# Performance work log

Hardware: AMD Instinct MI355X
Metric: run time of the kernel (lower is better)

## Reference

```python
import jax, jax.numpy as jnp
import numpy as np

N = 100000   # nodes
E = 1600000  # edges (avg degree 16)
D = 128      # feature width (constant across the 3 blocks)
L = 3        # number of residual LEConv blocks
EPS = 1e-5
SLOPE = 0.01  # leaky_relu negative slope


def setup_inputs() -> dict:
    key = jax.random.key(0)
    ks = jax.random.split(key, 10)
    y = jax.random.normal(ks[0], (N, D), dtype=jnp.float32)
    edge_index = jax.random.randint(ks[1], (2, E), 0, N, dtype=jnp.int64)
    s = 0.05
    W1 = jax.random.normal(ks[2], (L, D, D), dtype=jnp.float32) * s
    b1 = jax.random.normal(ks[3], (L, D), dtype=jnp.float32) * s
    W2 = jax.random.normal(ks[4], (L, D, D), dtype=jnp.float32) * s   # lin2: no bias
    W3 = jax.random.normal(ks[5], (L, D, D), dtype=jnp.float32) * s
    b3 = jax.random.normal(ks[6], (L, D), dtype=jnp.float32) * s
    ln_w = jnp.ones((L, D), dtype=jnp.float32)
    ln_b = jnp.zeros((L, D), dtype=jnp.float32)
    return {"y": y, "edge_index": edge_index, "W1": W1, "b1": b1,
            "W2": W2, "W3": W3, "b3": b3, "ln_w": ln_w, "ln_b": ln_b}


def reference(y, edge_index, W1, b1, W2, W3, b3, ln_w, ln_b):
    n = y.shape[0]
    src, dst = edge_index[0], edge_index[1]
    # in-degree per destination node (edge_weight = 1)
    deg = jax.ops.segment_sum(jnp.ones((src.shape[0],), dtype=y.dtype), dst,
                              num_segments=n)  # [N]
    for l in range(L):
        # LEConv: out_i = sum_{j->i} (lin1(x)_j - lin2(x)_i) + lin3(x)_i
        a = y @ W1[l] + b1[l]          # [N, D] (lin1, with bias)
        b = y @ W2[l]                  # [N, D] (lin2, no bias)
        agg = jax.ops.segment_sum(a[src], dst, num_segments=n) - deg[:, None] * b
        h = agg + y @ W3[l] + b3[l]    # + lin3(x)
        # PyG LayerNorm mode='graph', batch=None: scalar mean/std over all elems
        h = h - h.mean()
        h = h / (h.std() + EPS)
        h = h * ln_w[l] + ln_b[l]
        # leaky_relu, dropout p=0 (no-op), identity residual
        h = jnp.where(h >= 0, h, SLOPE * h)
        y = y + h
    return y
```

## Files before the change

kernel.cpp:

```cpp
#include <hip/hip_runtime.h>
#include <hip/hip_bf16.h>
#include <math.h>

#define N_NODES 100000
#define N_EDGES 1600000
#define DF      128
#define EPSV    1e-5f
#define SLOPE   0.01f
#define M_TOT   (N_NODES * DF)

#define HG    512
#define EPB   (N_EDGES / HG)
#define NBIN  391

typedef __hip_bfloat16 bf16;
typedef __attribute__((ext_vector_type(8))) short short8;
typedef __attribute__((ext_vector_type(4))) float f32x4;

__global__ void k_detect(const unsigned int* __restrict__ yw32, int* __restrict__ flagp)
{
    __shared__ int cnt;
    if (threadIdx.x == 0) cnt = 0;
    __syncthreads();
    unsigned w = yw32[threadIdx.x];
    int e = (w >> 7) & 0xFF;
    if (e >= 96 && e <= 140) atomicAdd(&cnt, 1);
    __syncthreads();
    if (threadIdx.x == 0) flagp[0] = (cnt >= 150) ? 1 : 0;
}

__global__ void k_zero(int* __restrict__ p, int n)
{
    int i = blockIdx.x * 256 + threadIdx.x;
    if (i < n) p[i] = 0;
}

__device__ __forceinline__ void edge_decode(const int* __restrict__ ei, int e,
                                            int& s, int& d)
{
    bool is64 = ((ei[1] | ei[3] | ei[5] | ei[7]) == 0);
    if (is64) { s = ei[2 * e]; d = ei[2 * (N_EDGES + e)]; }
    else      { s = ei[e];     d = ei[N_EDGES + e];       }
}

__global__ __launch_bounds__(256) void k_hist(
    const void* __restrict__ yin, bf16* __restrict__ yw,
    const int* __restrict__ flagp, const int* __restrict__ ei,
    int* __restrict__ histG)
{
    __shared__ int h[NBIN];
    const int tid = threadIdx.x, b = blockIdx.x;
    for (int i = tid; i < NBIN; i += 256) h[i] = 0;
    __syncthreads();

    const int e0 = b * EPB;
    for (int e = e0 + tid; e < e0 + EPB; e += 256) {
        int s, d;
        edge_decode(ei, e, s, d);
        if ((unsigned)s < N_NODES && (unsigned)d < N_NODES)
            atomicAdd(&h[d >> 8], 1);
    }

    const int isbf = flagp[0];
    for (long t = (long)b * 256 + tid; t < (M_TOT / 8); t += (long)HG * 256) {
        float f[8];
        if (isbf) {
            uint4 v = reinterpret_cast<const uint4*>(yin)[t];
            const bf16* sp = reinterpret_cast<const bf16*>(&v);
#pragma unroll
            for (int j = 0; j < 8; ++j) f[j] = __bfloat162float(sp[j]);
        } else {
            float4 v0 = reinterpret_cast<const float4*>(yin)[2 * t];
            float4 v1 = reinterpret_cast<const float4*>(yin)[2 * t + 1];
            f[0] = v0.x; f[1] = v0.y; f[2] = v0.z; f[3] = v0.w;
            f[4] = v1.x; f[5] = v1.y; f[6] = v1.z; f[7] = v1.w;
        }
        uint4 ov;
        bf16* o = reinterpret_cast<bf16*>(&ov);
#pragma unroll
        for (int j = 0; j < 8; ++j) {
            float x = f[j];
            if (!isfinite(x)) x = 0.f;
            o[j] = __float2bfloat16(x);
        }
        reinterpret_cast<uint4*>(yw)[t] = ov;
    }

    __syncthreads();
    for (int i = tid; i < NBIN; i += 256) histG[i * HG + b] = h[i];
}

__global__ void k_hscan1(int* __restrict__ histG, int* __restrict__ binTotal)
{
    __shared__ int sc[512];
    const int bin = blockIdx.x, tid = threadIdx.x;
    int v = histG[bin * HG + tid];
    sc[tid] = v;
    __syncthreads();
    for (int off = 1; off < 512; off <<= 1) {
        int t = (tid >= off) ? sc[tid - off] : 0;
        __syncthreads();
        sc[tid] += t;
        __syncthreads();
    }
    histG[bin * HG + tid] = sc[tid] - v;
    if (tid == 511) binTotal[bin] = sc[511];
}

__global__ void k_hscan2(const int* __restrict__ binTotal, int* __restrict__ binStart)
{
    __shared__ int sc[512];
    int tid = threadIdx.x;
    int v = (tid < NBIN) ? binTotal[tid] : 0;
    sc[tid] = v;
    __syncthreads();
    for (int off = 1; off < 512; off <<= 1) {
        int t = (tid >= off) ? sc[tid - off] : 0;
        __syncthreads();
        sc[tid] += t;
        __syncthreads();
    }
    if (tid < NBIN) binStart[tid] = sc[tid] - v;
}

__global__ __launch_bounds__(256) void k_scatter(
    const int* __restrict__ ei, const int* __restrict__ histG,
    const int* __restrict__ binStart, int* __restrict__ binned)
{
    __shared__ int base[NBIN];
    __shared__ int cur[NBIN];
    const int tid = threadIdx.x, b = blockIdx.x;
    for (int i = tid; i < NBIN; i += 256) {
        base[i] = binStart[i] + histG[i * HG + b];
        cur[i]  = 0;
    }
    __syncthreads();

    const int e0 = b * EPB;
    for (int e = e0 + tid; e < e0 + EPB; e += 256) {
        int s, d;
        edge_decode(ei, e, s, d);
        if ((unsigned)s < N_NODES && (unsigned)d < N_NODES) {
            int bin = d >> 8;
            int r = atomicAdd(&cur[bin], 1);
            binned[base[bin] + r] = ((d & 255) << 17) | s;
        }
    }
}

__global__ __launch_bounds__(256) void k_bin(
    const int* __restrict__ binned, const int* __restrict__ binStart,
    const int* __restrict__ binTotal, int* __restrict__ edst,
    int* __restrict__ degcnt, int* __restrict__ offs)
{
    __shared__ int hloc[256];
    __shared__ int lofs[256];
    __shared__ int sc[256];
    const int bin = blockIdx.x, tid = threadIdx.x;
    const int bbase = binStart[bin], cnt = binTotal[bin];

    hloc[tid] = 0;
    __syncthreads();
    for (int i = tid; i < cnt; i += 256)
        atomicAdd(&hloc[binned[bbase + i] >> 17], 1);
    __syncthreads();

    const int deg = hloc[tid];
    sc[tid] = deg;
    __syncthreads();
    for (int off = 1; off < 256; off <<= 1) {
        int t = (tid >= off) ? sc[tid - off] : 0;
        __syncthreads();
        sc[tid] += t;
        __syncthreads();
    }
    const int ex = sc[tid] - deg;
    lofs[tid] = ex;
    const int node = bin * 256 + tid;
    if (node < N_NODES) {
        degcnt[node] = deg;
        offs[node]   = bbase + ex;
    }
    hloc[tid] = 0;
    __syncthreads();

    for (int i = tid; i < cnt; i += 256) {
        int v = binned[bbase + i];
        int n = v >> 17;
        int r = atomicAdd(&hloc[n], 1);
        edst[bbase + lofs[n] + r] = v & 0x1FFFF;
    }
}

__global__ void k_wt(const void* __restrict__ W1, const void* __restrict__ W2,
                     const void* __restrict__ W3, bf16* __restrict__ Wt,
                     const int* __restrict__ flagp)
{
    int idx = blockIdx.x * 256 + threadIdx.x;
    const int isbf = flagp[0];
    int mat = idx >> 14;
    int r   = idx & 16383;
    int k   = r >> 7, n = r & 127;
    int l = mat / 3, which = mat - l * 3;
    const void* src = (which == 0) ? W1 : (which == 1 ? W2 : W3);
    size_t ofs = (size_t)l * 16384 + (size_t)k * 128 + n;
    float v = isbf ? __bfloat162float(reinterpret_cast<const bf16*>(src)[ofs])
                   : reinterpret_cast<const float*>(src)[ofs];
    if (!isfinite(v)) v = 0.f;
    Wt[((size_t)mat << 14) + (size_t)n * 128 + k] = __float2bfloat16(v);
}

__global__ void k_small(const void* __restrict__ b1, const void* __restrict__ b3,
                        const void* __restrict__ lnw, const void* __restrict__ lnb,
                        bf16* __restrict__ prm, const int* __restrict__ flagp)
{
    int i = blockIdx.x * 256 + threadIdx.x;
    if (i >= 1536) return;
    const int isbf = flagp[0];
    int which = i / 384, r = i - which * 384;
    const void* src = (which == 0) ? b1 : (which == 1) ? b3 : (which == 2) ? lnw : lnb;
    float v = isbf ? __bfloat162float(reinterpret_cast<const bf16*>(src)[r])
                   : reinterpret_cast<const float*>(src)[r];
    if (!isfinite(v)) v = 0.f;
    prm[i] = __float2bfloat16(v);
}

__global__ __launch_bounds__(256) void k_gemm3(
    bf16* __restrict__ yw, const bf16* __restrict__ hprev,
    const float* __restrict__ stats, const bf16* __restrict__ Wt,
    const bf16* __restrict__ prm, const int* __restrict__ degcnt,
    bf16* __restrict__ aBuf, bf16* __restrict__ cmb, int layer)
{
    __shared__ bf16 Asm[64][136];
    __shared__ bf16 Bsm[128][136];

    const int tid = threadIdx.x;
    const long r0 = (long)blockIdx.x * 64;

    const uint4* gy = reinterpret_cast<const uint4*>(yw);

    if (layer == 0) {
#pragma unroll
        for (int it = 0; it < 4; ++it) {
            int chunk = it * 256 + tid;
            int row = chunk >> 4, colc = (chunk & 15) * 8;
            uint4 v = make_uint4(0, 0, 0, 0);
            long grow = r0 + row;
            if (grow < N_NODES) v = gy[grow * 16 + (chunk & 15)];
            *reinterpret_cast<uint4*>(&Asm[row][colc]) = v;
        }
    } else {
        const float mean = stats[(layer - 1) * 2];
        const float inv  = stats[(layer - 1) * 2 + 1];
        const bf16* lnwc = prm + 768  + (layer - 1) * 128;
        const bf16* lnbc = prm + 1152 + (layer - 1) * 128;
        const uint4* gh = reinterpret_cast<const uint4*>(hprev);
#pragma unroll
        for (int it = 0; it < 4; ++it) {
            int chunk = it * 256 + tid;
            int row = chunk >> 4, c16 = chunk & 15, colc = c16 * 8;
            long grow = r0 + row;
            uint4 ov = make_uint4(0, 0, 0, 0);
            if (grow < N_NODES) {
                uint4 hv = gh[grow * 16 + c16];
                uint4 yv = gy[grow * 16 + c16];
                const bf16* h8 = reinterpret_cast<const bf16*>(&hv);
                const bf16* y8 = reinterpret_cast<const bf16*>(&yv);
                bf16* o8 = reinterpret_cast<bf16*>(&ov);
#pragma unroll
                for (int jj = 0; jj < 8; ++jj) {
                    float g = __bfloat162float(lnwc[colc + jj]);
                    float b = __bfloat162float(lnbc[colc + jj]);
                    float hh = (__bfloat162float(h8[jj]) - mean) * inv * g + b;
                    hh = (hh >= 0.f) ? hh : SLOPE * hh;
                    o8[jj] = __float2bfloat16(__bfloat162float(y8[jj]) + hh);
                }
                reinterpret_cast<uint4*>(yw)[grow * 16 + c16] = ov;
            }
            *reinterpret_cast<uint4*>(&Asm[row][colc]) = ov;
        }
    }

#define STAGE_B(MATIDX)                                                          \
    {                                                                            \
        const uint4* gw = reinterpret_cast<const uint4*>(Wt + ((size_t)(MATIDX) << 14)); \
        _Pragma("unroll")                                                        \
        for (int it = 0; it < 8; ++it) {                                         \
            int chunk = it * 256 + tid;                                          \
            *reinterpret_cast<uint4*>(&Bsm[chunk >> 4][(chunk & 15) * 8]) = gw[chunk]; \
        }                                                                        \
    }

    const int wave = tid >> 6, lane = tid & 63;
    const int lm = lane & 15, quad = lane >> 4;
    const int mrow = wave * 16 + lm;

    f32x4 accB[8], accC[8];
#pragma unroll
    for (int nt = 0; nt < 8; ++nt) {
        accB[nt] = (f32x4){0.f, 0.f, 0.f, 0.f};
        accC[nt] = (f32x4){0.f, 0.f, 0.f, 0.f};
    }

    STAGE_B(layer * 3 + 1);
    __syncthreads();
#pragma unroll
    for (int kk = 0; kk < 4; ++kk) {
        const int kb = kk * 32 + quad * 8;
        short8 afr = *reinterpret_cast<const short8*>(&Asm[mrow][kb]);
#pragma unroll
        for (int nt = 0; nt < 8; ++nt) {
            short8 bfr = *reinterpret_cast<const short8*>(&Bsm[nt * 16 + lm][kb]);
            accB[nt] = __builtin_amdgcn_mfma_f32_16x16x32_bf16(afr, bfr, accB[nt], 0, 0, 0);
        }
    }
    __syncthreads();

    STAGE_B(layer * 3 + 2);
    __syncthreads();
#pragma unroll
    for (int kk = 0; kk < 4; ++kk) {
        const int kb = kk * 32 + quad * 8;
        short8 afr = *reinterpret_cast<const short8*>(&Asm[mrow][kb]);
#pragma unroll
        for (int nt = 0; nt < 8; ++nt) {
            short8 bfr = *reinterpret_cast<const short8*>(&Bsm[nt * 16 + lm][kb]);
            accC[nt] = __builtin_amdgcn_mfma_f32_16x16x32_bf16(afr, bfr, accC[nt], 0, 0, 0);
        }
    }

    const bf16* b3c = prm + 384 + layer * 128;
#pragma unroll
    for (int i = 0; i < 4; ++i) {
        long row = r0 + wave * 16 + quad * 4 + i;
        if (row < N_NODES) {
            float degf = (float)degcnt[row];
#pragma unroll
            for (int nt = 0; nt < 8; ++nt) {
                int col = nt * 16 + lm;
                float v = accC[nt][i] + __bfloat162float(b3c[col]) - degf * accB[nt][i];
                cmb[row * 128 + col] = __float2bfloat16(v);
            }
        }
    }
    __syncthreads();

    STAGE_B(layer * 3 + 0);
    __syncthreads();
#pragma unroll
    for (int nt = 0; nt < 8; ++nt) accB[nt] = (f32x4){0.f, 0.f, 0.f, 0.f};
#pragma unroll
    for (int kk = 0; kk < 4; ++kk) {
        const int kb = kk * 32 + quad * 8;
        short8 afr = *reinterpret_cast<const short8*>(&Asm[mrow][kb]);
#pragma unroll
        for (int nt = 0; nt < 8; ++nt) {
            short8 bfr = *reinterpret_cast<const short8*>(&Bsm[nt * 16 + lm][kb]);
            accB[nt] = __builtin_amdgcn_mfma_f32_16x16x32_bf16(afr, bfr, accB[nt], 0, 0, 0);
        }
    }
    const bf16* b1c = prm + layer * 128;
#pragma unroll
    for (int i = 0; i < 4; ++i) {
        long row = r0 + wave * 16 + quad * 4 + i;
        if (row < N_NODES) {
#pragma unroll
            for (int nt = 0; nt < 8; ++nt) {
                int col = nt * 16 + lm;
                aBuf[row * 128 + col] =
                    __float2bfloat16(accB[nt][i] + __bfloat162float(b1c[col]));
            }
        }
    }
#undef STAGE_B
}

#define AGG_BLOCKS 2048
#define AGG_WAVES  (AGG_BLOCKS * 4)

__global__ __launch_bounds__(256, 8) void k_agg(
    const bf16* __restrict__ aBuf, bf16* __restrict__ cmb,
    const int* __restrict__ offs, const int* __restrict__ degcnt,
    const int* __restrict__ edst, float* __restrict__ buckets, int layer)
{
    const int tid  = threadIdx.x;
    const int lane = tid & 63;
    const int el   = lane >> 4;
    const int fb   = lane & 15;
    const int wid  = __builtin_amdgcn_readfirstlane((int)(blockIdx.x * 4) + (tid >> 6));

    const uint4* A4 = reinterpret_cast<const uint4*>(aBuf);

    float s1w = 0.f, s2w = 0.f;

#define ACC8(v)                                                                \
    {                                                                          \
        const unsigned* _u = reinterpret_cast<const unsigned*>(&(v));          \
        _Pragma("unroll")                                                      \
        for (int _d = 0; _d < 4; ++_d) {                                       \
            acc[2 * _d]     += __uint_as_float(_u[_d] << 16);                  \
            acc[2 * _d + 1] += __uint_as_float(_u[_d] & 0xffff0000u);          \
        }                                                                      \
    }

    for (int node = wid; node < N_NODES; node += AGG_WAVES) {
        const int start = offs[node];
        const int deg   = degcnt[node];

        const uint4 cv = reinterpret_cast<const uint4*>(cmb)[(size_t)node * 16 + fb];

        float acc[8];
#pragma unroll
        for (int i = 0; i < 8; ++i) acc[i] = 0.f;

        int j = el;
        for (; j + 12 < deg; j += 16) {
            int e0 = edst[start + j];
            int e1 = edst[start + j + 4];
            int e2 = edst[start + j + 8];
            int e3 = edst[start + j + 12];
            uint4 v0 = A4[(size_t)e0 * 16 + fb];
            uint4 v1 = A4[(size_t)e1 * 16 + fb];
            uint4 v2 = A4[(size_t)e2 * 16 + fb];
            uint4 v3 = A4[(size_t)e3 * 16 + fb];
            ACC8(v0); ACC8(v1); ACC8(v2); ACC8(v3);
        }
        if (j + 4 < deg) {
            int e0 = edst[start + j];
            int e1 = edst[start + j + 4];
            uint4 v0 = A4[(size_t)e0 * 16 + fb];
            uint4 v1 = A4[(size_t)e1 * 16 + fb];
            ACC8(v0); ACC8(v1);
            j += 8;
        }
        if (j < deg) {
            int e0 = edst[start + j];
            uint4 v0 = A4[(size_t)e0 * 16 + fb];
            ACC8(v0);
        }

#pragma unroll
        for (int i = 0; i < 8; ++i) {
            acc[i] += __shfl_xor(acc[i], 16);
            acc[i] += __shfl_xor(acc[i], 32);
        }

        const unsigned* cu = reinterpret_cast<const unsigned*>(&cv);
        float h[8];
#pragma unroll
        for (int d = 0; d < 4; ++d) {
            h[2 * d]     = acc[2 * d]     + __uint_as_float(cu[d] << 16);
            h[2 * d + 1] = acc[2 * d + 1] + __uint_as_float(cu[d] & 0xffff0000u);
        }
        uint4 ov;
        bf16* o8 = reinterpret_cast<bf16*>(&ov);
#pragma unroll
        for (int i = 0; i < 8; ++i) {
            o8[i] = __float2bfloat16(h[i]);
            s1w += h[i];
            s2w += h[i] * h[i];
        }
        if (el == 0) reinterpret_cast<uint4*>(cmb)[(size_t)node * 16 + fb] = ov;
    }
#undef ACC8

#pragma unroll
    for (int m = 1; m < 16; m <<= 1) {
        s1w += __shfl_xor(s1w, m);
        s2w += __shfl_xor(s2w, m);
    }
    if (lane == 0) {
        int bkt = wid & 255;
        atomicAdd(&buckets[layer * 512 + bkt * 2],     s1w);
        atomicAdd(&buckets[layer * 512 + bkt * 2 + 1], s2w);
    }
}

__global__ void k_red(const float* __restrict__ buckets, float* __restrict__ statsOut, int layer)
{
    __shared__ double red[8];
    const int tid = threadIdx.x;
    double s1 = (double)buckets[layer * 512 + tid * 2];
    double s2 = (double)buckets[layer * 512 + tid * 2 + 1];
#pragma unroll
    for (int m = 1; m < 64; m <<= 1) {
        s1 += __shfl_xor(s1, m);
        s2 += __shfl_xor(s2, m);
    }
    const int wv = tid >> 6;
    if ((tid & 63) == 0) { red[wv] = s1; red[4 + wv] = s2; }
    __syncthreads();
    if (tid == 0) {
        double S1 = red[0] + red[1] + red[2] + red[3];
        double S2 = red[4] + red[5] + red[6] + red[7];
        double mean, inv;
        if (isfinite(S1) && isfinite(S2)) {
            const double M = (double)M_TOT;
            mean = S1 / M;
            double var = S2 / M - mean * mean;
            if (!(var > 0.0)) var = 0.0;
            inv = 1.0 / (sqrt(var) + (double)EPSV);
        } else {
            mean = 0.0; inv = 1.0;
        }
        statsOut[layer * 2]     = (float)mean;
        statsOut[layer * 2 + 1] = (float)inv;
    }
}

__global__ __launch_bounds__(256) void k_norm(
    const bf16* __restrict__ hBuf, bf16* __restrict__ yw,
    const float* __restrict__ statsOut, const bf16* __restrict__ prm,
    void* __restrict__ outFinal, const int* __restrict__ flagp, int layer)
{
    const long i = (long)blockIdx.x * 256 + threadIdx.x;
    const float mean  = statsOut[layer * 2];
    const float scale = statsOut[layer * 2 + 1];

    uint4 hv = reinterpret_cast<const uint4*>(hBuf)[i];
    uint4 yv = reinterpret_cast<const uint4*>(yw)[i];
    const bf16* h8 = reinterpret_cast<const bf16*>(&hv);
    const bf16* y8 = reinterpret_cast<const bf16*>(&yv);
    const int colb = ((int)(i & 15)) * 8;
    const bf16* lnwc = prm + 768  + layer * 128;
    const bf16* lnbc = prm + 1152 + layer * 128;

    float r[8];
    uint4 ov;
    bf16* o8 = reinterpret_cast<bf16*>(&ov);
#pragma unroll
    for (int jj = 0; jj < 8; ++jj) {
        float g = __bfloat162float(lnwc[colb + jj]);
        float b = __bfloat162float(lnbc[colb + jj]);
        float h = (__bfloat162float(h8[jj]) - mean) * scale * g + b;
        h = (h >= 0.f) ? h : SLOPE * h;
        r[jj] = __bfloat162float(y8[jj]) + h;
        o8[jj] = __float2bfloat16(r[jj]);
    }
    if (flagp[0]) {
        reinterpret_cast<uint4*>(outFinal)[i] = ov;
    } else {
        float4 lo = make_float4(r[0], r[1], r[2], r[3]);
        float4 hi = make_float4(r[4], r[5], r[6], r[7]);
        reinterpret_cast<float4*>(outFinal)[2 * i]     = lo;
        reinterpret_cast<float4*>(outFinal)[2 * i + 1] = hi;
    }
}

extern "C" void kernel_launch(void* const* d_in, const int* in_sizes, int n_in,
                              void* d_out, int out_size, void* d_ws, size_t ws_size,
                              hipStream_t stream)
{
    const void* yIn = d_in[0];
    const int*  ei  = (const int*)d_in[1];
    const void* W1  = d_in[2];
    const void* b1  = d_in[3];
    const void* W2  = d_in[4];
    const void* W3  = d_in[5];
    const void* b3  = d_in[6];
    const void* lnw = d_in[7];
    const void* lnb = d_in[8];

    char* ws = (char*)d_ws;
    size_t o = 0;
    auto alloc = [&](size_t bytes) -> char* {
        char* p = ws + o;
        o += (bytes + 255) & ~(size_t)255;
        return p;
    };
    bf16* yw     = (bf16*)alloc((size_t)M_TOT * 2);
    bf16* aBuf   = (bf16*)alloc((size_t)M_TOT * 2);
    bf16* cmb    = (bf16*)alloc((size_t)M_TOT * 2);
    bf16* Wt     = (bf16*)alloc((size_t)9 * 16384 * 2);
    bf16* prm    = (bf16*)alloc((size_t)1536 * 2);
    int*  edst   = (int*)alloc((size_t)N_EDGES * 4);
    int*  binned = (int*)alloc((size_t)N_EDGES * 4);
    int*  histG  = (int*)alloc((size_t)NBIN * HG * 4);
    int*  binTot = (int*)alloc((size_t)NBIN * 4);
    int*  binSta = (int*)alloc((size_t)NBIN * 4);
    int*  offs   = (int*)alloc((size_t)N_NODES * 4);
    int*  degcnt = (int*)alloc((size_t)N_NODES * 4);
    const int nz = 3 * 512 + 8 + 8;
    int* zr = (int*)alloc((size_t)nz * 4);
    float* buckets  = (float*)zr;
    float* statsOut = (float*)(zr + 3 * 512);
    int*   flagp    = zr + 3 * 512 + 8;

    k_zero   <<<(nz + 255) / 256, 256, 0, stream>>>(zr, nz);
    k_detect <<<1, 256, 0, stream>>>((const unsigned int*)yIn, flagp);
    k_hist   <<<HG, 256, 0, stream>>>(yIn, yw, flagp, ei, histG);
    k_hscan1 <<<NBIN, 512, 0, stream>>>(histG, binTot);
    k_hscan2 <<<1, 512, 0, stream>>>(binTot, binSta);
    k_scatter<<<HG, 256, 0, stream>>>(ei, histG, binSta, binned);
    k_bin    <<<NBIN, 256, 0, stream>>>(binned, binSta, binTot, edst, degcnt, offs);
    k_wt     <<<(9 * 16384) / 256, 256, 0, stream>>>(W1, W2, W3, Wt, flagp);
    k_small  <<<6, 256, 0, stream>>>(b1, b3, lnw, lnb, prm, flagp);

    const int ngemm = (N_NODES + 63) / 64;
    for (int l = 0; l < 3; ++l) {
        k_gemm3<<<ngemm, 256, 0, stream>>>(yw, cmb, statsOut, Wt, prm, degcnt, aBuf, cmb, l);
        k_agg  <<<AGG_BLOCKS, 256, 0, stream>>>(aBuf, cmb, offs, degcnt, edst, buckets, l);
        k_red  <<<1, 256, 0, stream>>>(buckets, statsOut, l);
    }
    k_norm<<<M_TOT / (8 * 256), 256, 0, stream>>>(cmb, yw, statsOut, prm, d_out, flagp, 2);
}
```

Baseline: 492.9 us.

## Fold small setup and stats-reduction kernels into neighbours to cut launches

Removes the k_zero, k_hscan2, k_small and k_red launches. Bucket zeroing moves into k_detect, the bin-total scan into every k_scatter block, the bias/LN param conversion into an extra k_wt block, and the mean/std reduction into the prologue of each consumer block (k_gemm3, k_norm). Each consumer block now redundantly reduces 512 buckets in double precision and each scatter block redoes a 512-wide scan. AGG_BLOCKS is also doubled.

Measured after the change: 498.1 us. About the same (+1.1%).

```diff
diff --git a/kernel.cpp b/kernel.cpp
--- a/kernel.cpp
+++ b/kernel.cpp
@@ -17,22 +17,19 @@
 typedef __attribute__((ext_vector_type(8))) short short8;
 typedef __attribute__((ext_vector_type(4))) float f32x4;
 
-__global__ void k_detect(const unsigned int* __restrict__ yw32, int* __restrict__ flagp)
+__global__ void k_detect(const unsigned int* __restrict__ yw32, int* __restrict__ flagp,
+                         int* __restrict__ bucketsI)
 {
     __shared__ int cnt;
-    if (threadIdx.x == 0) cnt = 0;
-    __syncthreads();
-    unsigned w = yw32[threadIdx.x];
+    const int tid = threadIdx.x;
+    if (tid == 0) cnt = 0;
+    for (int i = tid; i < 1536; i += 256) bucketsI[i] = 0;
+    __syncthreads();
+    unsigned w = yw32[tid];
     int e = (w >> 7) & 0xFF;
     if (e >= 96 && e <= 140) atomicAdd(&cnt, 1);
     __syncthreads();
-    if (threadIdx.x == 0) flagp[0] = (cnt >= 150) ? 1 : 0;
-}
-
-__global__ void k_zero(int* __restrict__ p, int n)
-{
-    int i = blockIdx.x * 256 + threadIdx.x;
-    if (i < n) p[i] = 0;
+    if (tid == 0) flagp[0] = (cnt >= 150) ? 1 : 0;
 }
 
 __device__ __forceinline__ void edge_decode(const int* __restrict__ ei, int e,
@@ -107,32 +104,34 @@
     if (tid == 511) binTotal[bin] = sc[511];
 }
 
-__global__ void k_hscan2(const int* __restrict__ binTotal, int* __restrict__ binStart)
-{
-    __shared__ int sc[512];
-    int tid = threadIdx.x;
-    int v = (tid < NBIN) ? binTotal[tid] : 0;
-    sc[tid] = v;
-    __syncthreads();
-    for (int off = 1; off < 512; off <<= 1) {
-        int t = (tid >= off) ? sc[tid - off] : 0;
-        __syncthreads();
-        sc[tid] += t;
-        __syncthreads();
-    }
-    if (tid < NBIN) binStart[tid] = sc[tid] - v;
-}
-
 __global__ __launch_bounds__(256) void k_scatter(
     const int* __restrict__ ei, const int* __restrict__ histG,
-    const int* __restrict__ binStart, int* __restrict__ binned)
-{
+    const int* __restrict__ binTotal, int* __restrict__ binStart,
+    int* __restrict__ binned)
+{
+    __shared__ int sc[512];
     __shared__ int base[NBIN];
     __shared__ int cur[NBIN];
     const int tid = threadIdx.x, b = blockIdx.x;
+
+    {
+        int v0 = (tid < NBIN) ? binTotal[tid] : 0;
+        int v1 = (tid + 256 < NBIN) ? binTotal[tid + 256] : 0;
+        sc[tid] = v0; sc[tid + 256] = v1;
+        __syncthreads();
+        for (int off = 1; off < 512; off <<= 1) {
+            int a  = (tid >= off) ? sc[tid - off] : 0;
+            int b2 = (tid + 256 >= off) ? sc[tid + 256 - off] : 0;
+            __syncthreads();
+            sc[tid] += a; sc[tid + 256] += b2;
+            __syncthreads();
+        }
+    }
     for (int i = tid; i < NBIN; i += 256) {
-        base[i] = binStart[i] + histG[i * HG + b];
+        int ex = sc[i] - binTotal[i];
+        base[i] = ex + histG[i * HG + b];
         cur[i]  = 0;
+        if (b == 0) binStart[i] = ex;
     }
     __syncthreads();
 
@@ -194,10 +193,24 @@
 
 __global__ void k_wt(const void* __restrict__ W1, const void* __restrict__ W2,
                      const void* __restrict__ W3, bf16* __restrict__ Wt,
-                     const int* __restrict__ flagp)
-{
+                     const void* __restrict__ b1, const void* __restrict__ b3,
+                     const void* __restrict__ lnw, const void* __restrict__ lnb,
+                     bf16* __restrict__ prm, const int* __restrict__ flagp)
+{
+    const int isbf = flagp[0];
+    if (blockIdx.x == 576) {
+        for (int i = threadIdx.x; i < 1536; i += 256) {
+            int which = i / 384, r = i - which * 384;
+            const void* src = (which == 0) ? b1 : (which == 1) ? b3
+                            : (which == 2) ? lnw : lnb;
+            float v = isbf ? __bfloat162float(reinterpret_cast<const bf16*>(src)[r])
+                           : reinterpret_cast<const float*>(src)[r];
+            if (!isfinite(v)) v = 0.f;
+            prm[i] = __float2bfloat16(v);
+        }
+        return;
+    }
     int idx = blockIdx.x * 256 + threadIdx.x;
-    const int isbf = flagp[0];
     int mat = idx >> 14;
     int r   = idx & 16383;
     int k   = r >> 7, n = r & 127;
@@ -210,29 +223,49 @@
     Wt[((size_t)mat << 14) + (size_t)n * 128 + k] = __float2bfloat16(v);
 }
 
-__global__ void k_small(const void* __restrict__ b1, const void* __restrict__ b3,
-                        const void* __restrict__ lnw, const void* __restrict__ lnb,
-                        bf16* __restrict__ prm, const int* __restrict__ flagp)
-{
-    int i = blockIdx.x * 256 + threadIdx.x;
-    if (i >= 1536) return;
-    const int isbf = flagp[0];
-    int which = i / 384, r = i - which * 384;
-    const void* src = (which == 0) ? b1 : (which == 1) ? b3 : (which == 2) ? lnw : lnb;
-    float v = isbf ? __bfloat162float(reinterpret_cast<const bf16*>(src)[r])
-                   : reinterpret_cast<const float*>(src)[r];
-    if (!isfinite(v)) v = 0.f;
-    prm[i] = __float2bfloat16(v);
+__device__ __forceinline__ void stats_reduce(
+    const float* __restrict__ buckets, int layer, int tid,
+    double* redS, float* s_mean, float* s_inv)
+{
+    double s1 = (double)buckets[layer * 512 + tid * 2];
+    double s2 = (double)buckets[layer * 512 + tid * 2 + 1];
+#pragma unroll
+    for (int m = 1; m < 64; m <<= 1) {
+        s1 += __shfl_xor(s1, m);
+        s2 += __shfl_xor(s2, m);
+    }
+    const int wv = tid >> 6;
+    if ((tid & 63) == 0) { redS[wv] = s1; redS[4 + wv] = s2; }
+    __syncthreads();
+    if (tid == 0) {
+        double S1 = redS[0] + redS[1] + redS[2] + redS[3];
+        double S2 = redS[4] + redS[5] + redS[6] + redS[7];
+        double mean, inv;
+        if (isfinite(S1) && isfinite(S2)) {
+            const double M = (double)M_TOT;
+            mean = S1 / M;
+            double var = S2 / M - mean * mean;
+            if (!(var > 0.0)) var = 0.0;
+            inv = 1.0 / (sqrt(var) + (double)EPSV);
+        } else {
+            mean = 0.0; inv = 1.0;
+        }
+        *s_mean = (float)mean;
+        *s_inv  = (float)inv;
+    }
+    __syncthreads();
 }
 
 __global__ __launch_bounds__(256) void k_gemm3(
     bf16* __restrict__ yw, const bf16* __restrict__ hprev,
-    const float* __restrict__ stats, const bf16* __restrict__ Wt,
+    const float* __restrict__ buckets, const bf16* __restrict__ Wt,
     const bf16* __restrict__ prm, const int* __restrict__ degcnt,
     bf16* __restrict__ aBuf, bf16* __restrict__ cmb, int layer)
 {
     __shared__ bf16 Asm[64][136];
     __shared__ bf16 Bsm[128][136];
+    __shared__ double redS[8];
+    __shared__ float s_mean, s_inv;
 
     const int tid = threadIdx.x;
     const long r0 = (long)blockIdx.x * 64;
@@ -250,8 +283,9 @@
             *reinterpret_cast<uint4*>(&Asm[row][colc]) = v;
         }
     } else {
-        const float mean = stats[(layer - 1) * 2];
-        const float inv  = stats[(layer - 1) * 2 + 1];
+        stats_reduce(buckets, layer - 1, tid, redS, &s_mean, &s_inv);
+        const float mean = s_mean;
+        const float inv  = s_inv;
         const bf16* lnwc = prm + 768  + (layer - 1) * 128;
         const bf16* lnbc = prm + 1152 + (layer - 1) * 128;
         const uint4* gh = reinterpret_cast<const uint4*>(hprev);
@@ -375,7 +409,7 @@
 #undef STAGE_B
 }
 
-#define AGG_BLOCKS 2048
+#define AGG_BLOCKS 4096
 #define AGG_WAVES  (AGG_BLOCKS * 4)
 
 __global__ __launch_bounds__(256, 8) void k_agg(
@@ -476,46 +510,19 @@
     }
 }
 
-__global__ void k_red(const float* __restrict__ buckets, float* __restrict__ statsOut, int layer)
-{
-    __shared__ double red[8];
-    const int tid = threadIdx.x;
-    double s1 = (double)buckets[layer * 512 + tid * 2];
-    double s2 = (double)buckets[layer * 512 + tid * 2 + 1];
-#pragma unroll
-    for (int m = 1; m < 64; m <<= 1) {
-        s1 += __shfl_xor(s1, m);
-        s2 += __shfl_xor(s2, m);
-    }
-    const int wv = tid >> 6;
-    if ((tid & 63) == 0) { red[wv] = s1; red[4 + wv] = s2; }
-    __syncthreads();
-    if (tid == 0) {
-        double S1 = red[0] + red[1] + red[2] + red[3];
-        double S2 = red[4] + red[5] + red[6] + red[7];
-        double mean, inv;
-        if (isfinite(S1) && isfinite(S2)) {
-            const double M = (double)M_TOT;
-            mean = S1 / M;
-            double var = S2 / M - mean * mean;
-            if (!(var > 0.0)) var = 0.0;
-            inv = 1.0 / (sqrt(var) + (double)EPSV);
-        } else {
-            mean = 0.0; inv = 1.0;
-        }
-        statsOut[layer * 2]     = (float)mean;
-        statsOut[layer * 2 + 1] = (float)inv;
-    }
-}
-
 __global__ __launch_bounds__(256) void k_norm(
     const bf16* __restrict__ hBuf, bf16* __restrict__ yw,
-    const float* __restrict__ statsOut, const bf16* __restrict__ prm,
+    const float* __restrict__ buckets, const bf16* __restrict__ prm,
     void* __restrict__ outFinal, const int* __restrict__ flagp, int layer)
 {
-    const long i = (long)blockIdx.x * 256 + threadIdx.x;
-    const float mean  = statsOut[layer * 2];
-    const float scale = statsOut[layer * 2 + 1];
+    __shared__ double redS[8];
+    __shared__ float s_mean, s_inv;
+    const int tid = threadIdx.x;
+    stats_reduce(buckets, layer, tid, redS, &s_mean, &s_inv);
+    const float mean  = s_mean;
+    const float scale = s_inv;
+
+    const long i = (long)blockIdx.x * 256 + tid;
 
     uint4 hv = reinterpret_cast<const uint4*>(hBuf)[i];
     uint4 yv = reinterpret_cast<const uint4*>(yw)[i];
@@ -580,27 +587,22 @@
     int*  binSta = (int*)alloc((size_t)NBIN * 4);
     int*  offs   = (int*)alloc((size_t)N_NODES * 4);
     int*  degcnt = (int*)alloc((size_t)N_NODES * 4);
-    const int nz = 3 * 512 + 8 + 8;
+    const int nz = 3 * 512 + 8;
     int* zr = (int*)alloc((size_t)nz * 4);
-    float* buckets  = (float*)zr;
-    float* statsOut = (float*)(zr + 3 * 512);
-    int*   flagp    = zr + 3 * 512 + 8;
-
-    k_zero   <<<(nz + 255) / 256, 256, 0, stream>>>(zr, nz);
-    k_detect <<<1, 256, 0, stream>>>((const unsigned int*)yIn, flagp);
+    float* buckets = (float*)zr;
+    int*   flagp   = zr + 3 * 512;
+
+    k_detect <<<1, 256, 0, stream>>>((const unsigned int*)yIn, flagp, zr);
     k_hist   <<<HG, 256, 0, stream>>>(yIn, yw, flagp, ei, histG);
     k_hscan1 <<<NBIN, 512, 0, stream>>>(histG, binTot);
-    k_hscan2 <<<1, 512, 0, stream>>>(binTot, binSta);
-    k_scatter<<<HG, 256, 0, stream>>>(ei, histG, binSta, binned);
+    k_scatter<<<HG, 256, 0, stream>>>(ei, histG, binTot, binSta, binned);
     k_bin    <<<NBIN, 256, 0, stream>>>(binned, binSta, binTot, edst, degcnt, offs);
-    k_wt     <<<(9 * 16384) / 256, 256, 0, stream>>>(W1, W2, W3, Wt, flagp);
-    k_small  <<<6, 256, 0, stream>>>(b1, b3, lnw, lnb, prm, flagp);
+    k_wt     <<<577, 256, 0, stream>>>(W1, W2, W3, Wt, b1, b3, lnw, lnb, prm, flagp);
 
     const int ngemm = (N_NODES + 63) / 64;
     for (int l = 0; l < 3; ++l) {
-        k_gemm3<<<ngemm, 256, 0, stream>>>(yw, cmb, statsOut, Wt, prm, degcnt, aBuf, cmb, l);
+        k_gemm3<<<ngemm, 256, 0, stream>>>(yw, cmb, buckets, Wt, prm, degcnt, aBuf, cmb, l);
         k_agg  <<<AGG_BLOCKS, 256, 0, stream>>>(aBuf, cmb, offs, degcnt, edst, buckets, l);
-        k_red  <<<1, 256, 0, stream>>>(buckets, statsOut, l);
-    }
-    k_norm<<<M_TOT / (8 * 256), 256, 0, stream>>>(cmb, yw, statsOut, prm, d_out, flagp, 2);
-}
+    }
+    k_norm<<<M_TOT / (8 * 256), 256, 0, stream>>>(cmb, yw, buckets, prm, d_out, flagp, 2);
+}
```
